# Optimization experiments

Measured on AMD Instinct MI355X. Metric: run time of the kernel, lower is better.

Reference implementation:

```python
import jax, jax.numpy as jnp
import numpy as np

B, N_N, N_A, D = 1024, 96, 96, 512


def _normalize(x):
    return x / jnp.linalg.norm(x, axis=-1, keepdims=True)


def setup_inputs() -> dict:
    key = jax.random.key(0)
    ks = jax.random.split(key, 8)
    img_embs = _normalize(jax.random.normal(ks[0], (B, D), jnp.float32))
    normal_text_embs = _normalize(jax.random.normal(ks[1], (N_N, D), jnp.float32))
    abnormal_text_embs = _normalize(jax.random.normal(ks[2], (N_A, D), jnp.float32))
    logit_scale = jnp.full((1,), np.log(100.0), jnp.float32)  # CLIP temperature
    W1 = jax.random.normal(ks[3], (2 * D, D), jnp.float32) / np.sqrt(2 * D)
    b1 = jnp.zeros((D,), jnp.float32)
    W2 = jax.random.normal(ks[4], (D, D // 2), jnp.float32) / np.sqrt(D)
    b2 = jnp.zeros((D // 2,), jnp.float32)
    W3 = jax.random.normal(ks[5], (D // 2, D // 4), jnp.float32) / np.sqrt(D // 2)
    b3 = jnp.zeros((D // 4,), jnp.float32)
    return {"img_embs": img_embs, "normal_text_embs": normal_text_embs,
            "abnormal_text_embs": abnormal_text_embs, "logit_scale": logit_scale,
            "W1": W1, "b1": b1, "W2": W2, "b2": b2, "W3": W3, "b3": b3}


def _mlp(x, W1, b1, W2, b2, W3, b3):
    h = jax.nn.relu(x @ W1 + b1)
    h = jax.nn.relu(h @ W2 + b2)
    return h @ W3 + b3


def _branch(img_embs, text_embs, scale, W1, b1, W2, b2, W3, b3):
    # sims: [B, N]; softmax weights then exp-scaled text embeddings
    sims = (img_embs @ text_embs.T) * scale
    w = jax.nn.softmax(sims, axis=-1)
    scaled_text = text_embs[None, :, :] * jnp.exp(w)[:, :, None]      # [B, N, D]
    rep_img = jnp.broadcast_to(img_embs[:, None, :], scaled_text.shape)  # [B, N, D]
    x = jnp.concatenate([rep_img, scaled_text], axis=-1)              # [B, N, 2D]
    h = _mlp(x, W1, b1, W2, b2, W3, b3)                               # [B, N, D//4]
    return h.mean(axis=1)                                             # [B, D//4]


def reference(img_embs, normal_text_embs, abnormal_text_embs, logit_scale,
              W1, b1, W2, b2, W3, b3):
    scale = jnp.exp(logit_scale[0])
    h_n = _branch(img_embs, normal_text_embs, scale, W1, b1, W2, b2, W3, b3)
    h_a = _branch(img_embs, abnormal_text_embs, scale, W1, b1, W2, b2, W3, b3)
    return (h_n, h_a)
```

## Files before the change

kernel.cpp:

```cpp
#include <hip/hip_runtime.h>
#include <hip/hip_bf16.h>


typedef __attribute__((ext_vector_type(8))) short short8;
typedef __attribute__((ext_vector_type(4))) float floatx4;
typedef __attribute__((ext_vector_type(4))) unsigned int uint4v;

__device__ __forceinline__ unsigned short f2bf(float x) {
    unsigned int u = __float_as_uint(x);
    u += 0x7fffu + ((u >> 16) & 1u);
    return (unsigned short)(u >> 16);
}
__device__ __forceinline__ float bf2f(unsigned short u) {
    return __uint_as_float(((unsigned int)u) << 16);
}

template <bool BF16OUT>
__device__ __forceinline__ void gemm64(
    const float* __restrict__ A0, const float* __restrict__ A1, int rows0,
    const float* __restrict__ Bm, float* __restrict__ Cf,
    unsigned short* __restrict__ Cb, int bx, int by,
    unsigned char* smem, int t) {
    float (*sAT)[68] = (float (*)[68])smem;
    int r0b = bx * 64, c0b = by * 64;
    int rg = t >> 4, cg = t & 15;
    int c0 = c0b + cg * 4;
    float acc[4][4];
#pragma unroll
    for (int r = 0; r < 4; r++)
#pragma unroll
        for (int c = 0; c < 4; c++) acc[r][c] = 0.f;

    for (int k0 = 0; k0 < 512; k0 += 32) {
#pragma unroll
        for (int i = 0; i < 2; i++) {
            int row = (t >> 3) + i * 32;
            int kk = (t & 7) * 4;
            int gr = r0b + row;
            const float* Ap = (gr < rows0) ? (A0 + gr * 512) : (A1 + (gr - rows0) * 512);
            float4 av = *(const float4*)(Ap + k0 + kk);
            sAT[kk + 0][row] = av.x; sAT[kk + 1][row] = av.y;
            sAT[kk + 2][row] = av.z; sAT[kk + 3][row] = av.w;
        }
        __syncthreads();
#pragma unroll
        for (int kk = 0; kk < 32; kk++) {
            float4 a = *(const float4*)(&sAT[kk][rg * 4]);
            float4 bv = *(const float4*)(Bm + (k0 + kk) * 512 + c0);
            float ar[4] = {a.x, a.y, a.z, a.w};
            float bc[4] = {bv.x, bv.y, bv.z, bv.w};
#pragma unroll
            for (int r = 0; r < 4; r++)
#pragma unroll
                for (int c = 0; c < 4; c++)
                    acc[r][c] = fmaf(ar[r], bc[c], acc[r][c]);
        }
        __syncthreads();
    }
    int r0 = r0b + rg * 4;
#pragma unroll
    for (int r = 0; r < 4; r++) {
        if (BF16OUT) {
            unsigned long long pk =
                (unsigned long long)f2bf(acc[r][0]) |
                ((unsigned long long)f2bf(acc[r][1]) << 16) |
                ((unsigned long long)f2bf(acc[r][2]) << 32) |
                ((unsigned long long)f2bf(acc[r][3]) << 48);
            *(unsigned long long*)(Cb + (r0 + r) * 512 + c0) = pk;
        } else {
            *(float4*)(Cf + (r0 + r) * 512 + c0) =
                make_float4(acc[r][0], acc[r][1], acc[r][2], acc[r][3]);
        }
    }
}

__global__ __launch_bounds__(256) void prep_kernel(
    const float* __restrict__ img, const float* __restrict__ tn,
    const float* __restrict__ ta, const float* __restrict__ ls,
    const float* __restrict__ W1, const float* __restrict__ W2,
    float* __restrict__ e_ws, float* __restrict__ U_ws,
    unsigned short* __restrict__ Tb, unsigned short* __restrict__ W2T) {
    __shared__ __align__(16) unsigned char smem[9216];
    int idx = blockIdx.x;
    int t = threadIdx.x;

    if (idx < 1024) {
        int b = idx;
        float* sImg = (float*)smem;
        float* sS   = sImg + 512;
        float* sMx  = sS + 192;
        float* sSum = sMx + 2;
        for (int i = t; i < 512; i += 256) sImg[i] = img[b * 512 + i];
        __syncthreads();
        float scale = __expf(ls[0]);
        int g = t & 7;
#pragma unroll
        for (int i = 0; i < 6; i++) {
            int n = (t >> 3) + 32 * i;
            const float* tx = (n < 96) ? (tn + n * 512) : (ta + (n - 96) * 512);
            float d = 0.f;
#pragma unroll
            for (int s = 0; s < 16; s++) {
                int k = g * 4 + s * 32;
                float4 x = *(const float4*)(tx + k);
                d += x.x * sImg[k] + x.y * sImg[k + 1] + x.z * sImg[k + 2] + x.w * sImg[k + 3];
            }
            d += __shfl_xor(d, 1);
            d += __shfl_xor(d, 2);
            d += __shfl_xor(d, 4);
            if (g == 0) sS[n] = d * scale;
        }
        __syncthreads();
        if (t < 2) {
            float m = -1e30f;
            for (int n = 0; n < 96; n++) m = fmaxf(m, sS[t * 96 + n]);
            float s = 0.f;
            for (int n = 0; n < 96; n++) s += __expf(sS[t * 96 + n] - m);
            sMx[t] = m; sSum[t] = s;
        }
        __syncthreads();
        if (t < 192) {
            int br = t / 96, n = t % 96;
            float w = __expf(sS[t] - sMx[br]) / sSum[br];
            e_ws[(br * 1024 + b) * 96 + n] = __expf(w);
        }
    } else if (idx < 1152) {
        int i = idx - 1024;
        gemm64<false>(img, img, 1 << 20, W1, U_ws, nullptr, i & 15, i >> 4, smem, t);
    } else if (idx < 1176) {
        int i = idx - 1152;
        gemm64<true>(tn, ta, 96, W1 + 512 * 512, nullptr, Tb, i % 3, i / 3, smem, t);
    } else {
        int i = idx - 1176;
        int n0 = i * 64;
        for (int r = 0; r < 64; r++) {
            int n = n0 + r;
            for (int k = t; k < 512; k += 256)
                W2T[n * 512 + k] = f2bf(W2[k * 256 + n]);
        }
    }
}

__global__ __launch_bounds__(256, 2) void branch_mlp4(
    const float* __restrict__ U, const unsigned short* __restrict__ Tb,
    const float* __restrict__ e_all, const unsigned short* __restrict__ W2T,
    const float* __restrict__ b1, const float* __restrict__ b2,
    const float* __restrict__ W3, const float* __restrict__ b3,
    float* __restrict__ out) {
    int b = blockIdx.x, br = blockIdx.y;
    const unsigned short* T = Tb + br * (96 * 512);

    __shared__ float sUb[512];
    __shared__ float sE[96];
    __shared__ __align__(16) unsigned short sH[2][96][88];
    __shared__ float sM2[256];
    __shared__ float sPart[256];

    int t = threadIdx.x;
    for (int i = t; i < 512; i += 256) sUb[i] = U[b * 512 + i] + b1[i];
    if (t < 96) sE[t] = e_all[(br * 1024 + b) * 96 + t];
    __syncthreads();

    const int wave = t >> 6, lane = t & 63;
    const int frow = lane & 15, fkq = (lane >> 4) * 8;
    const int ncol0 = wave * 64;
    const int srow = t >> 3;
    const int skc = (t & 7) * 8;

    const floatx4 fz = {0.f, 0.f, 0.f, 0.f};
    floatx4 acc[6][4];
#pragma unroll
    for (int mt = 0; mt < 6; mt++)
#pragma unroll
        for (int j = 0; j < 4; j++) acc[mt][j] = fz;

    int trow[3]; float ev[3]; short8 tv[3];
#pragma unroll
    for (int i2 = 0; i2 < 3; i2++) {
        trow[i2] = srow + 32 * i2;
        ev[i2] = sE[trow[i2]];
        tv[i2] = *(const short8*)(T + trow[i2] * 512 + skc);
    }
    const unsigned short* Bbase = W2T + (ncol0 + frow) * 512 + fkq;
    short8 bpre[4];
#pragma unroll
    for (int j = 0; j < 4; j++)
        bpre[j] = *(const short8*)(Bbase + j * (16 * 512));

#pragma unroll
    for (int s = 0; s < 8; s++) {
        int k0 = s * 64;
        float4 u0 = *(const float4*)(&sUb[k0 + skc]);
        float4 u1 = *(const float4*)(&sUb[k0 + skc + 4]);
        float ua[8] = {u0.x, u0.y, u0.z, u0.w, u1.x, u1.y, u1.z, u1.w};
#pragma unroll
        for (int i2 = 0; i2 < 3; i2++) {
            uint4v pk;
#pragma unroll
            for (int jj = 0; jj < 4; jj++) {
                float f0 = fmaxf(fmaf(ev[i2], bf2f((unsigned short)tv[i2][2 * jj]), ua[2 * jj]), 0.f);
                float f1 = fmaxf(fmaf(ev[i2], bf2f((unsigned short)tv[i2][2 * jj + 1]), ua[2 * jj + 1]), 0.f);
                __hip_bfloat162 h2 = __float22bfloat162_rn(make_float2(f0, f1));
                unsigned int bits;
                __builtin_memcpy(&bits, &h2, 4);
                pk[jj] = bits;
            }
            *(uint4v*)(&sH[s & 1][trow[i2]][skc]) = pk;
        }
        short8 bcur0[4];
#pragma unroll
        for (int j = 0; j < 4; j++) bcur0[j] = bpre[j];
        if (s < 7) {
#pragma unroll
            for (int i2 = 0; i2 < 3; i2++)
                tv[i2] = *(const short8*)(T + trow[i2] * 512 + k0 + 64 + skc);
#pragma unroll
            for (int j = 0; j < 4; j++)
                bpre[j] = *(const short8*)(Bbase + j * (16 * 512) + k0 + 64);
        }
        __syncthreads();
        short8 b1f[4];
#pragma unroll
        for (int j = 0; j < 4; j++)
            b1f[j] = *(const short8*)(Bbase + j * (16 * 512) + k0 + 32);
#pragma unroll
        for (int mt = 0; mt < 6; mt++) {
            short8 afr = *(const short8*)(&sH[s & 1][mt * 16 + frow][fkq]);
#pragma unroll
            for (int j = 0; j < 4; j++)
                acc[mt][j] = __builtin_amdgcn_mfma_f32_16x16x32_bf16(afr, bcur0[j], acc[mt][j], 0, 0, 0);
        }
#pragma unroll
        for (int mt = 0; mt < 6; mt++) {
            short8 afr = *(const short8*)(&sH[s & 1][mt * 16 + frow][32 + fkq]);
#pragma unroll
            for (int j = 0; j < 4; j++)
                acc[mt][j] = __builtin_amdgcn_mfma_f32_16x16x32_bf16(afr, b1f[j], acc[mt][j], 0, 0, 0);
        }
    }

#pragma unroll
    for (int j = 0; j < 4; j++) {
        int col = ncol0 + j * 16 + frow;
        float bb = b2[col];
        float s = 0.f;
#pragma unroll
        for (int mt = 0; mt < 6; mt++)
#pragma unroll
            for (int r = 0; r < 4; r++)
                s += fmaxf(acc[mt][j][r] + bb, 0.f);
        s += __shfl_xor(s, 16);
        s += __shfl_xor(s, 32);
        if (lane < 16) sM2[col] = s * (1.0f / 96.0f);
    }
    __syncthreads();

    int col = t & 127, ks2 = t >> 7;
    const float* w3p = W3 + (ks2 * 128) * 128 + col;
    const float* mp = sM2 + ks2 * 128;
    float o = 0.f;
#pragma unroll 8
    for (int k = 0; k < 128; k++) o = fmaf(mp[k], w3p[k * 128], o);
    sPart[t] = o;
    __syncthreads();
    if (t < 128) out[(br * 1024 + b) * 128 + t] = sPart[t] + sPart[t + 128] + b3[t];
}

extern "C" void kernel_launch(void* const* d_in, const int* in_sizes, int n_in,
                              void* d_out, int out_size, void* d_ws, size_t ws_size,
                              hipStream_t stream) {
    const float* img = (const float*)d_in[0];
    const float* tn  = (const float*)d_in[1];
    const float* ta  = (const float*)d_in[2];
    const float* ls  = (const float*)d_in[3];
    const float* W1  = (const float*)d_in[4];
    const float* b1  = (const float*)d_in[5];
    const float* W2  = (const float*)d_in[6];
    const float* b2  = (const float*)d_in[7];
    const float* W3  = (const float*)d_in[8];
    const float* b3  = (const float*)d_in[9];
    float* out = (float*)d_out;
    float* ws  = (float*)d_ws;

    float* e_ws = ws;
    float* U_ws = ws + 196608;
    unsigned short* Tb  = (unsigned short*)(ws + 720896);
    unsigned short* W2T = (unsigned short*)(ws + 770048);

    prep_kernel<<<1180, 256, 0, stream>>>(img, tn, ta, ls, W1, W2, e_ws, U_ws, Tb, W2T);
    branch_mlp4<<<dim3(1024, 2), 256, 0, stream>>>(U_ws, Tb, e_ws, W2T, b1, b2, W3, b3, out);
}
```

Measured before the change: 206.0 us.

## Rework prep kernel tiling and widen branch MLP to 512 threads

```diff
diff --git a/kernel.cpp b/kernel.cpp
--- a/kernel.cpp
+++ b/kernel.cpp
@@ -16,60 +16,50 @@
 }
 
 template <bool BF16OUT>
-__device__ __forceinline__ void gemm64(
+__device__ __forceinline__ void gemm32(
     const float* __restrict__ A0, const float* __restrict__ A1, int rows0,
     const float* __restrict__ Bm, float* __restrict__ Cf,
-    unsigned short* __restrict__ Cb, int bx, int by,
-    unsigned char* smem, int t) {
-    float (*sAT)[68] = (float (*)[68])smem;
-    int r0b = bx * 64, c0b = by * 64;
+    unsigned short* __restrict__ Cb, int mt, int nt, float* sAT, int t) {
+    int r0 = mt * 32, c0 = nt * 64;
     int rg = t >> 4, cg = t & 15;
-    int c0 = c0b + cg * 4;
-    float acc[4][4];
-#pragma unroll
-    for (int r = 0; r < 4; r++)
+    int lrow = t >> 3, k4 = (t & 7) * 4;
+    int gr = r0 + lrow;
+    const float* Ap = (gr < rows0) ? (A0 + gr * 512) : (A1 + (gr - rows0) * 512);
+    float acc[2][4];
+#pragma unroll
+    for (int r = 0; r < 2; r++)
 #pragma unroll
         for (int c = 0; c < 4; c++) acc[r][c] = 0.f;
-
+    const float* Bp = Bm + c0 + cg * 4;
     for (int k0 = 0; k0 < 512; k0 += 32) {
-#pragma unroll
-        for (int i = 0; i < 2; i++) {
-            int row = (t >> 3) + i * 32;
-            int kk = (t & 7) * 4;
-            int gr = r0b + row;
-            const float* Ap = (gr < rows0) ? (A0 + gr * 512) : (A1 + (gr - rows0) * 512);
-            float4 av = *(const float4*)(Ap + k0 + kk);
-            sAT[kk + 0][row] = av.x; sAT[kk + 1][row] = av.y;
-            sAT[kk + 2][row] = av.z; sAT[kk + 3][row] = av.w;
-        }
-        __syncthreads();
-#pragma unroll
+        __syncthreads();
+        float4 av = *(const float4*)(Ap + k0 + k4);
+        sAT[(k4 + 0) * 34 + lrow] = av.x;
+        sAT[(k4 + 1) * 34 + lrow] = av.y;
+        sAT[(k4 + 2) * 34 + lrow] = av.z;
+        sAT[(k4 + 3) * 34 + lrow] = av.w;
+        __syncthreads();
+#pragma unroll 8
         for (int kk = 0; kk < 32; kk++) {
-            float4 a = *(const float4*)(&sAT[kk][rg * 4]);
-            float4 bv = *(const float4*)(Bm + (k0 + kk) * 512 + c0);
-            float ar[4] = {a.x, a.y, a.z, a.w};
-            float bc[4] = {bv.x, bv.y, bv.z, bv.w};
-#pragma unroll
-            for (int r = 0; r < 4; r++)
-#pragma unroll
-                for (int c = 0; c < 4; c++)
-                    acc[r][c] = fmaf(ar[r], bc[c], acc[r][c]);
-        }
-        __syncthreads();
-    }
-    int r0 = r0b + rg * 4;
-#pragma unroll
-    for (int r = 0; r < 4; r++) {
+            float a0 = sAT[kk * 34 + rg * 2];
+            float a1 = sAT[kk * 34 + rg * 2 + 1];
+            float4 bv = *(const float4*)(Bp + (k0 + kk) * 512);
+            acc[0][0] = fmaf(a0, bv.x, acc[0][0]); acc[0][1] = fmaf(a0, bv.y, acc[0][1]);
+            acc[0][2] = fmaf(a0, bv.z, acc[0][2]); acc[0][3] = fmaf(a0, bv.w, acc[0][3]);
+            acc[1][0] = fmaf(a1, bv.x, acc[1][0]); acc[1][1] = fmaf(a1, bv.y, acc[1][1]);
+            acc[1][2] = fmaf(a1, bv.z, acc[1][2]); acc[1][3] = fmaf(a1, bv.w, acc[1][3]);
+        }
+    }
+    int rr = r0 + rg * 2, cc = c0 + cg * 4;
+#pragma unroll
+    for (int r = 0; r < 2; r++) {
         if (BF16OUT) {
             unsigned long long pk =
-                (unsigned long long)f2bf(acc[r][0]) |
-                ((unsigned long long)f2bf(acc[r][1]) << 16) |
-                ((unsigned long long)f2bf(acc[r][2]) << 32) |
-                ((unsigned long long)f2bf(acc[r][3]) << 48);
-            *(unsigned long long*)(Cb + (r0 + r) * 512 + c0) = pk;
+                (unsigned long long)f2bf(acc[r][0]) | ((unsigned long long)f2bf(acc[r][1]) << 16) |
+                ((unsigned long long)f2bf(acc[r][2]) << 32) | ((unsigned long long)f2bf(acc[r][3]) << 48);
+            *(unsigned long long*)(Cb + (rr + r) * 512 + cc) = pk;
         } else {
-            *(float4*)(Cf + (r0 + r) * 512 + c0) =
-                make_float4(acc[r][0], acc[r][1], acc[r][2], acc[r][3]);
+            *(float4*)(Cf + (rr + r) * 512 + cc) = make_float4(acc[r][0], acc[r][1], acc[r][2], acc[r][3]);
         }
     }
 }
@@ -80,68 +70,103 @@
     const float* __restrict__ W1, const float* __restrict__ W2,
     float* __restrict__ e_ws, float* __restrict__ U_ws,
     unsigned short* __restrict__ Tb, unsigned short* __restrict__ W2T) {
-    __shared__ __align__(16) unsigned char smem[9216];
+    __shared__ __align__(16) float smem[8704];
     int idx = blockIdx.x;
     int t = threadIdx.x;
 
-    if (idx < 1024) {
-        int b = idx;
-        float* sImg = (float*)smem;
-        float* sS   = sImg + 512;
-        float* sMx  = sS + 192;
-        float* sSum = sMx + 2;
-        for (int i = t; i < 512; i += 256) sImg[i] = img[b * 512 + i];
+    if (idx < 256) {
+        int bi0 = idx * 4;
+        float* sImg = smem;
+        float* sS   = smem + 2064;
+        float* sMx  = smem + 2832;
+        float* sSum = smem + 2840;
+#pragma unroll
+        for (int p = 0; p < 2; p++) {
+            int i4 = t + 256 * p;
+            int i = i4 >> 7, k4 = (i4 & 127) * 4;
+            float4 v = *(const float4*)(img + (bi0 + i) * 512 + k4);
+            sImg[i * 516 + k4 + 0] = v.x; sImg[i * 516 + k4 + 1] = v.y;
+            sImg[i * 516 + k4 + 2] = v.z; sImg[i * 516 + k4 + 3] = v.w;
+        }
         __syncthreads();
         float scale = __expf(ls[0]);
-        int g = t & 7;
-#pragma unroll
-        for (int i = 0; i < 6; i++) {
-            int n = (t >> 3) + 32 * i;
-            const float* tx = (n < 96) ? (tn + n * 512) : (ta + (n - 96) * 512);
-            float d = 0.f;
-#pragma unroll
-            for (int s = 0; s < 16; s++) {
-                int k = g * 4 + s * 32;
-                float4 x = *(const float4*)(tx + k);
-                d += x.x * sImg[k] + x.y * sImg[k + 1] + x.z * sImg[k + 2] + x.w * sImg[k + 3];
-            }
-            d += __shfl_xor(d, 1);
-            d += __shfl_xor(d, 2);
-            d += __shfl_xor(d, 4);
-            if (g == 0) sS[n] = d * scale;
-        }
-        __syncthreads();
-        if (t < 2) {
+        int i = t & 3, n0 = (t >> 2) * 3;
+        const float* txp[3];
+#pragma unroll
+        for (int r = 0; r < 3; r++) {
+            int n = n0 + r;
+            txp[r] = (n < 96) ? (tn + n * 512) : (ta + (n - 96) * 512);
+        }
+        float d0 = 0.f, d1 = 0.f, d2 = 0.f;
+        const float* ib = &sImg[i * 516];
+#pragma unroll 4
+        for (int k4 = 0; k4 < 512; k4 += 4) {
+            float4 iv = *(const float4*)(ib + k4);
+            float4 a = *(const float4*)(txp[0] + k4);
+            float4 b = *(const float4*)(txp[1] + k4);
+            float4 c = *(const float4*)(txp[2] + k4);
+            d0 += iv.x * a.x + iv.y * a.y + iv.z * a.z + iv.w * a.w;
+            d1 += iv.x * b.x + iv.y * b.y + iv.z * b.z + iv.w * b.w;
+            d2 += iv.x * c.x + iv.y * c.y + iv.z * c.z + iv.w * c.w;
+        }
+        sS[i * 192 + n0 + 0] = d0 * scale;
+        sS[i * 192 + n0 + 1] = d1 * scale;
+        sS[i * 192 + n0 + 2] = d2 * scale;
+        __syncthreads();
+        if (t < 8) {
+            int ii = t >> 1, brx = t & 1;
+            const float* base = &sS[ii * 192 + brx * 96];
             float m = -1e30f;
-            for (int n = 0; n < 96; n++) m = fmaxf(m, sS[t * 96 + n]);
+            for (int n = 0; n < 96; n++) m = fmaxf(m, base[n]);
             float s = 0.f;
-            for (int n = 0; n < 96; n++) s += __expf(sS[t * 96 + n] - m);
+            for (int n = 0; n < 96; n++) s += __expf(base[n] - m);
             sMx[t] = m; sSum[t] = s;
         }
         __syncthreads();
-        if (t < 192) {
-            int br = t / 96, n = t % 96;
-            float w = __expf(sS[t] - sMx[br]) / sSum[br];
-            e_ws[(br * 1024 + b) * 96 + n] = __expf(w);
-        }
-    } else if (idx < 1152) {
-        int i = idx - 1024;
-        gemm64<false>(img, img, 1 << 20, W1, U_ws, nullptr, i & 15, i >> 4, smem, t);
-    } else if (idx < 1176) {
-        int i = idx - 1152;
-        gemm64<true>(tn, ta, 96, W1 + 512 * 512, nullptr, Tb, i % 3, i / 3, smem, t);
+#pragma unroll
+        for (int p = 0; p < 3; p++) {
+            int j = t + 256 * p;
+            int ii = j & 3, n = j >> 2;
+            int brx = (n >= 96) ? 1 : 0;
+            int nn = n - brx * 96;
+            float w = __expf(sS[ii * 192 + n] - sMx[ii * 2 + brx]) / sSum[ii * 2 + brx];
+            e_ws[(brx * 1024 + bi0 + ii) * 96 + nn] = __expf(w);
+        }
+    } else if (idx < 512) {
+        int i2 = idx - 256;
+        gemm32<false>(img, img, 1 << 20, W1, U_ws, nullptr, i2 >> 3, i2 & 7, smem, t);
+    } else if (idx < 560) {
+        int i2 = idx - 512;
+        gemm32<true>(tn, ta, 96, W1 + 512 * 512, nullptr, Tb, i2 >> 3, i2 & 7, smem, t);
     } else {
-        int i = idx - 1176;
-        int n0 = i * 64;
-        for (int r = 0; r < 64; r++) {
-            int n = n0 + r;
-            for (int k = t; k < 512; k += 256)
-                W2T[n * 512 + k] = f2bf(W2[k * 256 + n]);
-        }
-    }
-}
-
-__global__ __launch_bounds__(256, 2) void branch_mlp4(
+        int ci = idx - 560;
+        int k0 = ci * 32;
+        float* sWT = smem;
+        int kr = t >> 3, n0 = (t & 7) * 32;
+#pragma unroll
+        for (int c = 0; c < 8; c++) {
+            float4 v = *(const float4*)(W2 + (k0 + kr) * 256 + n0 + c * 4);
+            sWT[(n0 + c * 4 + 0) * 33 + kr] = v.x;
+            sWT[(n0 + c * 4 + 1) * 33 + kr] = v.y;
+            sWT[(n0 + c * 4 + 2) * 33 + kr] = v.z;
+            sWT[(n0 + c * 4 + 3) * 33 + kr] = v.w;
+        }
+        __syncthreads();
+        unsigned short pk[32];
+#pragma unroll
+        for (int k = 0; k < 32; k++) pk[k] = f2bf(sWT[t * 33 + k]);
+#pragma unroll
+        for (int g = 0; g < 4; g++) {
+            uint4v u;
+#pragma unroll
+            for (int c = 0; c < 4; c++)
+                u[c] = (unsigned int)pk[g * 8 + 2 * c] | ((unsigned int)pk[g * 8 + 2 * c + 1] << 16);
+            *(uint4v*)(W2T + t * 512 + k0 + g * 8) = u;
+        }
+    }
+}
+
+__global__ __launch_bounds__(512, 4) void branch_mlp5(
     const float* __restrict__ U, const unsigned short* __restrict__ Tb,
     const float* __restrict__ e_all, const unsigned short* __restrict__ W2T,
     const float* __restrict__ b1, const float* __restrict__ b2,
@@ -154,38 +179,36 @@
     __shared__ float sE[96];
     __shared__ __align__(16) unsigned short sH[2][96][88];
     __shared__ float sM2[256];
-    __shared__ float sPart[256];
+    __shared__ float sPart[512];
 
     int t = threadIdx.x;
-    for (int i = t; i < 512; i += 256) sUb[i] = U[b * 512 + i] + b1[i];
+    sUb[t] = U[b * 512 + t] + b1[t];
     if (t < 96) sE[t] = e_all[(br * 1024 + b) * 96 + t];
     __syncthreads();
 
     const int wave = t >> 6, lane = t & 63;
     const int frow = lane & 15, fkq = (lane >> 4) * 8;
-    const int ncol0 = wave * 64;
+    const int ncol0 = wave * 32;
     const int srow = t >> 3;
     const int skc = (t & 7) * 8;
+    const bool two = (srow < 32);
 
     const floatx4 fz = {0.f, 0.f, 0.f, 0.f};
-    floatx4 acc[6][4];
-#pragma unroll
-    for (int mt = 0; mt < 6; mt++)
-#pragma unroll
-        for (int j = 0; j < 4; j++) acc[mt][j] = fz;
-
-    int trow[3]; float ev[3]; short8 tv[3];
-#pragma unroll
-    for (int i2 = 0; i2 < 3; i2++) {
-        trow[i2] = srow + 32 * i2;
-        ev[i2] = sE[trow[i2]];
-        tv[i2] = *(const short8*)(T + trow[i2] * 512 + skc);
-    }
+    floatx4 acc[6][2];
+#pragma unroll
+    for (int mt = 0; mt < 6; mt++) {
+        acc[mt][0] = fz; acc[mt][1] = fz;
+    }
+
+    int trow1 = srow + 64;
+    float ev0 = sE[srow], ev1 = two ? sE[trow1] : 0.f;
+    short8 tv0 = *(const short8*)(T + srow * 512 + skc);
+    short8 tv1 = two ? *(const short8*)(T + trow1 * 512 + skc) : tv0;
+
     const unsigned short* Bbase = W2T + (ncol0 + frow) * 512 + fkq;
-    short8 bpre[4];
-#pragma unroll
-    for (int j = 0; j < 4; j++)
-        bpre[j] = *(const short8*)(Bbase + j * (16 * 512));
+    short8 bpre[2];
+    bpre[0] = *(const short8*)(Bbase);
+    bpre[1] = *(const short8*)(Bbase + 16 * 512);
 
 #pragma unroll
     for (int s = 0; s < 8; s++) {
@@ -193,54 +216,56 @@
         float4 u0 = *(const float4*)(&sUb[k0 + skc]);
         float4 u1 = *(const float4*)(&sUb[k0 + skc + 4]);
         float ua[8] = {u0.x, u0.y, u0.z, u0.w, u1.x, u1.y, u1.z, u1.w};
-#pragma unroll
-        for (int i2 = 0; i2 < 3; i2++) {
+        {
             uint4v pk;
 #pragma unroll
             for (int jj = 0; jj < 4; jj++) {
-                float f0 = fmaxf(fmaf(ev[i2], bf2f((unsigned short)tv[i2][2 * jj]), ua[2 * jj]), 0.f);
-                float f1 = fmaxf(fmaf(ev[i2], bf2f((unsigned short)tv[i2][2 * jj + 1]), ua[2 * jj + 1]), 0.f);
+                float f0 = fmaxf(fmaf(ev0, bf2f((unsigned short)tv0[2 * jj]), ua[2 * jj]), 0.f);
+                float f1 = fmaxf(fmaf(ev0, bf2f((unsigned short)tv0[2 * jj + 1]), ua[2 * jj + 1]), 0.f);
                 __hip_bfloat162 h2 = __float22bfloat162_rn(make_float2(f0, f1));
-                unsigned int bits;
-                __builtin_memcpy(&bits, &h2, 4);
+                unsigned int bits; __builtin_memcpy(&bits, &h2, 4);
                 pk[jj] = bits;
             }
-            *(uint4v*)(&sH[s & 1][trow[i2]][skc]) = pk;
-        }
-        short8 bcur0[4];
-#pragma unroll
-        for (int j = 0; j < 4; j++) bcur0[j] = bpre[j];
+            *(uint4v*)(&sH[s & 1][srow][skc]) = pk;
+        }
+        if (two) {
+            uint4v pk;
+#pragma unroll
+            for (int jj = 0; jj < 4; jj++) {
+                float f0 = fmaxf(fmaf(ev1, bf2f((unsigned short)tv1[2 * jj]), ua[2 * jj]), 0.f);
+                float f1 = fmaxf(fmaf(ev1, bf2f((unsigned short)tv1[2 * jj + 1]), ua[2 * jj + 1]), 0.f);
+                __hip_bfloat162 h2 = __float22bfloat162_rn(make_float2(f0, f1));
+                unsigned int bits; __builtin_memcpy(&bits, &h2, 4);
+                pk[jj] = bits;
+            }
+            *(uint4v*)(&sH[s & 1][trow1][skc]) = pk;
+        }
+        short8 bcur0 = bpre[0], bcur1 = bpre[1];
         if (s < 7) {
-#pragma unroll
-            for (int i2 = 0; i2 < 3; i2++)
-                tv[i2] = *(const short8*)(T + trow[i2] * 512 + k0 + 64 + skc);
-#pragma unroll
-            for (int j = 0; j < 4; j++)
-                bpre[j] = *(const short8*)(Bbase + j * (16 * 512) + k0 + 64);
-        }
-        __syncthreads();
-        short8 b1f[4];
-#pragma unroll
-        for (int j = 0; j < 4; j++)
-            b1f[j] = *(const short8*)(Bbase + j * (16 * 512) + k0 + 32);
+            tv0 = *(const short8*)(T + srow * 512 + k0 + 64 + skc);
+            if (two) tv1 = *(const short8*)(T + trow1 * 512 + k0 + 64 + skc);
+            bpre[0] = *(const short8*)(Bbase + k0 + 64);
+            bpre[1] = *(const short8*)(Bbase + 16 * 512 + k0 + 64);
+        }
+        __syncthreads();
+        short8 b1f0 = *(const short8*)(Bbase + k0 + 32);
+        short8 b1f1 = *(const short8*)(Bbase + 16 * 512 + k0 + 32);
 #pragma unroll
         for (int mt = 0; mt < 6; mt++) {
             short8 afr = *(const short8*)(&sH[s & 1][mt * 16 + frow][fkq]);
-#pragma unroll
-            for (int j = 0; j < 4; j++)
-                acc[mt][j] = __builtin_amdgcn_mfma_f32_16x16x32_bf16(afr, bcur0[j], acc[mt][j], 0, 0, 0);
+            acc[mt][0] = __builtin_amdgcn_mfma_f32_16x16x32_bf16(afr, bcur0, acc[mt][0], 0, 0, 0);
+            acc[mt][1] = __builtin_amdgcn_mfma_f32_16x16x32_bf16(afr, bcur1, acc[mt][1], 0, 0, 0);
         }
 #pragma unroll
         for (int mt = 0; mt < 6; mt++) {
             short8 afr = *(const short8*)(&sH[s & 1][mt * 16 + frow][32 + fkq]);
-#pragma unroll
-            for (int j = 0; j < 4; j++)
-                acc[mt][j] = __builtin_amdgcn_mfma_f32_16x16x32_bf16(afr, b1f[j], acc[mt][j], 0, 0, 0);
-        }
-    }
-
-#pragma unroll
-    for (int j = 0; j < 4; j++) {
+            acc[mt][0] = __builtin_amdgcn_mfma_f32_16x16x32_bf16(afr, b1f0, acc[mt][0], 0, 0, 0);
+            acc[mt][1] = __builtin_amdgcn_mfma_f32_16x16x32_bf16(afr, b1f1, acc[mt][1], 0, 0, 0);
+        }
+    }
+
+#pragma unroll
+    for (int j = 0; j < 2; j++) {
         int col = ncol0 + j * 16 + frow;
         float bb = b2[col];
         float s = 0.f;
@@ -255,15 +280,17 @@
     }
     __syncthreads();
 
-    int col = t & 127, ks2 = t >> 7;
-    const float* w3p = W3 + (ks2 * 128) * 128 + col;
-    const float* mp = sM2 + ks2 * 128;
+    int col = t & 127, kq = t >> 7;
+    const float* w3p = W3 + (kq * 64) * 128 + col;
+    const float* mp = sM2 + kq * 64;
     float o = 0.f;
 #pragma unroll 8
-    for (int k = 0; k < 128; k++) o = fmaf(mp[k], w3p[k * 128], o);
+    for (int k = 0; k < 64; k++) o = fmaf(mp[k], w3p[k * 128], o);
     sPart[t] = o;
     __syncthreads();
-    if (t < 128) out[(br * 1024 + b) * 128 + t] = sPart[t] + sPart[t + 128] + b3[t];
+    if (t < 128)
+        out[(br * 1024 + b) * 128 + t] =
+            sPart[t] + sPart[t + 128] + sPart[t + 256] + sPart[t + 384] + b3[t];
 }
 
 extern "C" void kernel_launch(void* const* d_in, const int* in_sizes, int n_in,
@@ -287,6 +314,6 @@
     unsigned short* Tb  = (unsigned short*)(ws + 720896);
     unsigned short* W2T = (unsigned short*)(ws + 770048);
 
-    prep_kernel<<<1180, 256, 0, stream>>>(img, tn, ta, ls, W1, W2, e_ws, U_ws, Tb, W2T);
-    branch_mlp4<<<dim3(1024, 2), 256, 0, stream>>>(U_ws, Tb, e_ws, W2T, b1, b2, W3, b3, out);
-}
+    prep_kernel<<<576, 256, 0, stream>>>(img, tn, ta, ls, W1, W2, e_ws, U_ws, Tb, W2T);
+    branch_mlp5<<<dim3(1024, 2), 512, 0, stream>>>(U_ws, Tb, e_ws, W2T, b1, b2, W3, b3, out);
+}
```

Measured after the change: 212.9 us. 1.03x slower.
